# Kernel tuning notes

Measured on AMD Instinct MI355X. Metric: run time of the kernel, lower is better.

The kernel has to match this reference:

```python
import jax, jax.numpy as jnp
from jax import lax
import numpy as np

HEADS = 8

def _hswish(x):
    return x * jnp.clip(x + 3.0, 0.0, 6.0) / 6.0

def _sep_conv(x, dw, pw, pad):
    # depthwise conv (groups=C) followed by 1x1 pointwise conv, no bias
    dn = ('NCHW', 'OIHW', 'NCHW')
    y = lax.conv_general_dilated(x, dw, (1, 1), [(pad, pad), (pad, pad)],
                                 dimension_numbers=dn, feature_group_count=x.shape[1])
    return lax.conv_general_dilated(y, pw, (1, 1), [(0, 0), (0, 0)], dimension_numbers=dn)

def _bn(x, g, b, m, v):
    # SyncBatchNorm in eval mode (running stats), eps=1e-5
    inv = g / jnp.sqrt(v + 1e-5)
    return (x - m[:, None, None]) * inv[:, None, None] + b[:, None, None]

def _gn(x, g, b, groups=2):
    B, C, H, W = x.shape
    xg = x.reshape(B, groups, -1)
    mu = xg.mean(-1, keepdims=True)
    var = xg.var(-1, keepdims=True)
    xg = (xg - mu) / jnp.sqrt(var + 1e-5)
    return xg.reshape(B, C, H, W) * g[:, None, None] + b[:, None, None]

def _ln(x, g, b):
    mu = x.mean(-1, keepdims=True)
    var = x.var(-1, keepdims=True)
    return (x - mu) / jnp.sqrt(var + 1e-5) * g + b

def _forward(fl, h, w):
    (x, ln_q_g, ln_q_b, ln_k_g, ln_k_b, ln_v_g, ln_v_b, w_q, w_k, w_v, w_proj, b_proj,
     dw0, pw0, gn_g, gn_b, dw1, pw1, dw2, pw2,
     bn0_g, bn0_b, bn0_m, bn0_v, bn1_g, bn1_b, bn1_m, bn1_v, bn2_g, bn2_b, bn2_m, bn2_v) = fl
    B, C, N = x.shape  # C = attr_num tokens, N = dim = h*w
    d = N // HEADS
    scale = d ** -0.5
    q = _ln(x, ln_q_g, ln_q_b) @ w_q.T
    k = _ln(x, ln_k_g, ln_k_b) @ w_k.T
    v = _ln(x, ln_v_g, ln_v_b) @ w_v.T

    def agg(t):
        # aggregator(t.transpose(1,2), (h,w)) then head split; net input is (B,C,h,w)
        img = t.reshape(B, C, h, w)
        p0, p1, p2, p3 = jnp.split(img, 4, axis=1)  # seg_dim = C//4
        x0 = _hswish(_bn(p0, bn0_g, bn0_b, bn0_m, bn0_v))
        x1 = _hswish(_bn(_sep_conv(p1, dw1, pw1, 1), bn1_g, bn1_b, bn1_m, bn1_v))
        x2 = _hswish(_bn(_sep_conv(p2, dw2, pw2, 2), bn2_g, bn2_b, bn2_m, bn2_v))
        xl = _hswish(_gn(_sep_conv(p3, dw0, pw0, 1), gn_g, gn_b))
        y = jnp.concatenate([x0, x1, x2, xl], axis=1).reshape(B, C, N)
        return y.reshape(B, C, HEADS, d).transpose(0, 2, 1, 3)  # (B,H,C,d)

    qh, kh, vh = agg(q), agg(k), agg(v)
    scores = jnp.einsum('bhcd,bhkd->bhck', qh, kh)
    attn = jax.nn.softmax(jax.nn.gelu(scores, approximate=False) * scale, axis=-1)
    out = jnp.einsum('bhck,bhkd->bhcd', attn, vh).reshape(B, C, N)  # raw reshape as in torch
    out = out @ w_proj.T + b_proj
    out = out / jnp.maximum(jnp.linalg.norm(out, axis=-1, keepdims=True), 1e-12)
    return out, attn


def setup_inputs() -> dict:
    key = jax.random.key(0)
    ks = jax.random.split(key, 12)
    B, C, N = 32, 312, 1024
    sd = C // 4  # 78
    f32 = jnp.float32
    rn = lambda k, shp, s: jax.random.normal(k, shp, f32) * s
    inp = {
        'x': rn(ks[0], (B, C, N), 1.0),
        'h': 32, 'w': 32,
        'ln_q_g': jnp.ones((N,), f32), 'ln_q_b': jnp.zeros((N,), f32),
        'ln_k_g': jnp.ones((N,), f32), 'ln_k_b': jnp.zeros((N,), f32),
        'ln_v_g': jnp.ones((N,), f32), 'ln_v_b': jnp.zeros((N,), f32),
        'w_q': rn(ks[1], (N, N), N ** -0.5),
        'w_k': rn(ks[2], (N, N), N ** -0.5),
        'w_v': rn(ks[3], (N, N), N ** -0.5),
        'w_proj': rn(ks[4], (N, N), N ** -0.5),
        'b_proj': jnp.zeros((N,), f32),
        'dw0': rn(ks[5], (sd, 1, 3, 3), 1.0 / 3.0),
        'pw0': rn(ks[6], (sd, sd, 1, 1), sd ** -0.5),
        'gn_g': jnp.ones((sd,), f32), 'gn_b': jnp.zeros((sd,), f32),
        'dw1': rn(ks[7], (sd, 1, 3, 3), 1.0 / 3.0),
        'pw1': rn(ks[8], (sd, sd, 1, 1), sd ** -0.5),
        'dw2': rn(ks[9], (sd, 1, 5, 5), 1.0 / 5.0),
        'pw2': rn(ks[10], (sd, sd, 1, 1), sd ** -0.5),
    }
    for i in range(3):
        inp[f'bn{i}_g'] = jnp.ones((sd,), f32)
        inp[f'bn{i}_b'] = jnp.zeros((sd,), f32)
        inp[f'bn{i}_m'] = jnp.zeros((sd,), f32)
        inp[f'bn{i}_v'] = jnp.ones((sd,), f32)
    return inp


def reference(x, h, w, ln_q_g, ln_q_b, ln_k_g, ln_k_b, ln_v_g, ln_v_b, w_q, w_k, w_v, w_proj, b_proj, dw0, pw0, gn_g, gn_b, dw1, pw1, dw2, pw2, bn0_g, bn0_b, bn0_m, bn0_v, bn1_g, bn1_b, bn1_m, bn1_v, bn2_g, bn2_b, bn2_m, bn2_v):
    fl = (x, ln_q_g, ln_q_b, ln_k_g, ln_k_b, ln_v_g, ln_v_b, w_q, w_k, w_v, w_proj, b_proj,
          dw0, pw0, gn_g, gn_b, dw1, pw1, dw2, pw2,
          bn0_g, bn0_b, bn0_m, bn0_v, bn1_g, bn1_b, bn1_m, bn1_v, bn2_g, bn2_b, bn2_m, bn2_v)
    return _forward(fl, h, w)
```

## Files before the change

### kernel.cpp

```cpp
#include <hip/hip_runtime.h>
#include <hip/hip_bf16.h>
#include <float.h>

typedef __hip_bfloat16 bf16;
typedef __attribute__((ext_vector_type(8))) __bf16 bfrag;
typedef __attribute__((ext_vector_type(4))) float f32x4;

#define B_ 32
#define C_ 312
#define N_ 1024
#define H_ 8
#define D_ 128
#define SD_ 78
#define BC_ (B_ * C_)
#define BH_ (B_ * H_)

__device__ __forceinline__ float bf2f(bf16 x) { return __bfloat162float(x); }
__device__ __forceinline__ bf16 f2bf(float x) { return __float2bfloat16(x); }
__device__ __forceinline__ float hswish(float x) {
    return x * fminf(fmaxf(x + 3.0f, 0.0f), 6.0f) * (1.0f / 6.0f);
}

__device__ __forceinline__ void gload_lds16(const void* g, void* l) {
    __builtin_amdgcn_global_load_lds(
        (const __attribute__((address_space(1))) void*)g,
        (__attribute__((address_space(3))) void*)l, 16, 0, 0);
}

__global__ void ln_kernel(const float* __restrict__ x, bf16* __restrict__ xn) {
    int r = blockIdx.x;
    int t = threadIdx.x;
    const float* xr = x + (size_t)r * N_;
    float4 v4 = *reinterpret_cast<const float4*>(xr + t * 4);
    float s = v4.x + v4.y + v4.z + v4.w;
    float sq = v4.x * v4.x + v4.y * v4.y + v4.z * v4.z + v4.w * v4.w;
    __shared__ float rs[256], rq[256];
    rs[t] = s; rq[t] = sq; __syncthreads();
    for (int o = 128; o > 0; o >>= 1) {
        if (t < o) { rs[t] += rs[t + o]; rq[t] += rq[t + o]; }
        __syncthreads();
    }
    float mu = rs[0] * (1.0f / N_);
    float var = rq[0] * (1.0f / N_) - mu * mu;
    float rstd = rsqrtf(var + 1e-5f);
    __bf16 o4[4] = { (__bf16)((v4.x - mu) * rstd), (__bf16)((v4.y - mu) * rstd),
                     (__bf16)((v4.z - mu) * rstd), (__bf16)((v4.w - mu) * rstd) };
    *reinterpret_cast<uint2*>(reinterpret_cast<__bf16*>(xn) + (size_t)r * N_ + t * 4) =
        *reinterpret_cast<const uint2*>(o4);
}

__global__ void wcvt_kernel(const float* __restrict__ wq, const float* __restrict__ wk,
                            const float* __restrict__ wv, const float* __restrict__ wp,
                            const float* __restrict__ gq, const float* __restrict__ bq,
                            const float* __restrict__ gk, const float* __restrict__ bk,
                            const float* __restrict__ gv, const float* __restrict__ bv_,
                            bf16* __restrict__ wqkv, float* __restrict__ bias3,
                            bf16* __restrict__ wpb) {
    int n = blockIdx.x;
    int t = threadIdx.x;
    int k4 = t * 4;
    const float* src; const float* G = nullptr; const float* Bv = nullptr;
    if (n < 1024)      { src = wq + (size_t)n * N_;          G = gq; Bv = bq; }
    else if (n < 2048) { src = wk + (size_t)(n - 1024) * N_; G = gk; Bv = bk; }
    else if (n < 3072) { src = wv + (size_t)(n - 2048) * N_; G = gv; Bv = bv_; }
    else               { src = wp + (size_t)(n - 3072) * N_; }
    float4 w4 = *reinterpret_cast<const float4*>(src + k4);
    if (G) {
        __bf16 o[4] = { (__bf16)(w4.x * G[k4]),     (__bf16)(w4.y * G[k4 + 1]),
                        (__bf16)(w4.z * G[k4 + 2]), (__bf16)(w4.w * G[k4 + 3]) };
        *reinterpret_cast<uint2*>(wqkv + (size_t)n * N_ + k4) = *reinterpret_cast<const uint2*>(o);
        float s = w4.x * Bv[k4] + w4.y * Bv[k4 + 1] + w4.z * Bv[k4 + 2] + w4.w * Bv[k4 + 3];
        __shared__ float rs[256];
        rs[t] = s; __syncthreads();
        for (int o2 = 128; o2 > 0; o2 >>= 1) {
            if (t < o2) rs[t] += rs[t + o2];
            __syncthreads();
        }
        if (t == 0) bias3[n] = rs[0];
    } else {
        __bf16 o[4] = { (__bf16)w4.x, (__bf16)w4.y, (__bf16)w4.z, (__bf16)w4.w };
        *reinterpret_cast<uint2*>(wpb + (size_t)(n - 3072) * N_ + k4) = *reinterpret_cast<const uint2*>(o);
    }
}

template <bool OUTF32>
__global__ __launch_bounds__(256) void mfma_gemm_bw(
        const bf16* __restrict__ A_,
        const bf16* __restrict__ Wb,
        const float* __restrict__ bias, int nTx,
        void* __restrict__ O0, void* __restrict__ O1, void* __restrict__ O2) {
    const int K = 1024, Nout = 1024;
    __shared__ __bf16 sA[128 * 64];
    __shared__ __bf16 sB[128 * 64];
    const __bf16* A = reinterpret_cast<const __bf16*>(A_);
    const __bf16* W = reinterpret_cast<const __bf16*>(Wb);

    int t = threadIdx.x;
    int lane = t & 63, wave = t >> 6;
    int wm = (wave >> 1) * 64, wn = (wave & 1) * 64;
    int quad = lane >> 4, l15 = lane & 15;

    int cpx = gridDim.x >> 3;
    int tile = (blockIdx.x & 7) * cpx + (blockIdx.x >> 3);
    int bx = tile % nTx, by = tile / nTx;
    int m0 = by * 128;
    int w0 = bx * 128;
    int which = bx >> 3;
    int n0 = (bx & 7) * 128;

    int rowLoc = wave * 8 + (lane >> 3);
    int c8s = (lane & 7) ^ (lane >> 3);
    const __bf16* gA = A + (size_t)(m0 + rowLoc) * K + c8s * 8;
    const __bf16* gW = W + (size_t)(w0 + rowLoc) * K + c8s * 8;

    f32x4 acc[4][4];
#pragma unroll
    for (int i = 0; i < 4; i++)
#pragma unroll
        for (int j = 0; j < 4; j++) acc[i][j] = (f32x4)(0.f);

    for (int kt = 0; kt < 16; kt++) {
        int k0 = kt * 64;
#pragma unroll
        for (int cc = 0; cc < 4; cc++) {
            gload_lds16(gA + (size_t)cc * 32 * K + k0, &sA[cc * 2048 + wave * 512]);
            gload_lds16(gW + (size_t)cc * 32 * K + k0, &sB[cc * 2048 + wave * 512]);
        }
        __syncthreads();
#pragma unroll
        for (int kk = 0; kk < 2; kk++) {
            bfrag af[4], bfr[4];
#pragma unroll
            for (int mt = 0; mt < 4; mt++) {
                int row = wm + mt * 16 + l15;
                af[mt] = *reinterpret_cast<const bfrag*>(
                    &sA[(row * 8 + ((kk * 4 + quad) ^ (row & 7))) * 8]);
            }
#pragma unroll
            for (int nt = 0; nt < 4; nt++) {
                int row = wn + nt * 16 + l15;
                bfr[nt] = *reinterpret_cast<const bfrag*>(
                    &sB[(row * 8 + ((kk * 4 + quad) ^ (row & 7))) * 8]);
            }
#pragma unroll
            for (int mt = 0; mt < 4; mt++)
#pragma unroll
                for (int nt = 0; nt < 4; nt++)
                    acc[mt][nt] = __builtin_amdgcn_mfma_f32_16x16x32_bf16(af[mt], bfr[nt], acc[mt][nt], 0, 0, 0);
        }
        __syncthreads();
    }
    void* Cout = which == 0 ? O0 : (which == 1 ? O1 : O2);
#pragma unroll
    for (int mt = 0; mt < 4; mt++) {
#pragma unroll
        for (int nt = 0; nt < 4; nt++) {
            int cloc = wn + nt * 16 + l15;
            float bb = bias ? bias[w0 + cloc] : 0.f;
            int col = n0 + cloc;
#pragma unroll
            for (int r = 0; r < 4; r++) {
                int row = m0 + wm + mt * 16 + quad * 4 + r;
                float v = acc[mt][nt][r] + bb;
                if (OUTF32) ((float*)Cout)[(size_t)row * Nout + col] = v;
                else        ((bf16*)Cout)[(size_t)row * Nout + col] = f2bf(v);
            }
        }
    }
}

__global__ void seg0_kernel(const bf16* __restrict__ t0, const bf16* __restrict__ t1,
                            const bf16* __restrict__ t2,
                            bf16* __restrict__ h0, bf16* __restrict__ h1,
                            bf16* __restrict__ h2,
                            const float* __restrict__ g, const float* __restrict__ b,
                            const float* __restrict__ m, const float* __restrict__ v) {
    int ti = blockIdx.y;
    const bf16* tin = ti == 0 ? t0 : (ti == 1 ? t1 : t2);
    bf16* th = ti == 0 ? h0 : (ti == 1 ? h1 : h2);
    int bc = blockIdx.x;
    int bi = bc / SD_, c = bc % SD_;
    float inv = g[c] * rsqrtf(v[c] + 1e-5f);
    float mm = m[c], bb = b[c];
    const __bf16* tp = reinterpret_cast<const __bf16*>(tin) + ((size_t)bi * C_ + c) * N_;
    __bf16* base = reinterpret_cast<__bf16*>(th) + (size_t)bi * H_ * C_ * D_;
    int n = threadIdx.x * 4;
    uint2 in2 = *reinterpret_cast<const uint2*>(tp + n);
    const __bf16* iv = reinterpret_cast<const __bf16*>(&in2);
    __bf16 o4[4];
#pragma unroll
    for (int j = 0; j < 4; j++)
        o4[j] = (__bf16)hswish(((float)iv[j] - mm) * inv + bb);
    *reinterpret_cast<uint2*>(&base[((n >> 7) * C_ + c) * D_ + (n & 127)]) =
        *reinterpret_cast<const uint2*>(o4);
}

template <int KS, int MODE>
__device__ __forceinline__ void dwpw_impl(
        char* uMem, float* sDwF, float* sWk,
        const bf16* __restrict__ tin, int cOff,
        const float* __restrict__ dw, const float* __restrict__ pw,
        const float* __restrict__ g, const float* __restrict__ b,
        const float* __restrict__ m, const float* __restrict__ v,
        bf16* __restrict__ th, float* __restrict__ rawOut,
        int r0, int bi, int tid) {
    constexpr int WKP = ((KS * KS + 3) / 4) * 4;
    __bf16* sIn = reinterpret_cast<__bf16*>(uMem);
    float (*sWt)[80] = reinterpret_cast<float (*)[80]>(uMem);
    const int P = KS / 2;

    for (int u = tid; u < SD_ * KS * 2; u += 512) {
        int rowi = u >> 1, side = u & 1;
        *reinterpret_cast<uint2*>(sIn + rowi * 40 + (side ? 36 : 0)) = make_uint2(0u, 0u);
    }
    const __bf16* tbase = reinterpret_cast<const __bf16*>(tin) + ((size_t)bi * C_ + cOff) * N_;
    for (int u = tid; u < SD_ * KS * 4; u += 512) {
        int c = u / (KS * 4);
        int rem = u - c * (KS * 4);
        int di = rem >> 2, cb = rem & 3;
        int ii = r0 + di - P;
        uint4 val = make_uint4(0u, 0u, 0u, 0u);
        if (ii >= 0 && ii <= 31)
            val = *reinterpret_cast<const uint4*>(tbase + (size_t)c * N_ + ii * 32 + cb * 8);
        __bf16* dst = sIn + (c * KS + di) * 40 + 4 + cb * 8;
        *reinterpret_cast<uint2*>(dst)     = make_uint2(val.x, val.y);
        *reinterpret_cast<uint2*>(dst + 4) = make_uint2(val.z, val.w);
    }
    for (int i = tid; i < SD_ * KS * KS; i += 512) {
        int c = i / (KS * KS), q = i - c * (KS * KS);
        sWk[c * WKP + q] = dw[i];
    }
    __syncthreads();

    for (int u = tid; u < SD_ * 4; u += 512) {
        int c = u >> 2, q8 = (u & 3) << 3;
        const __bf16* rbase = sIn + (size_t)(c * KS) * 40;
        __bf16 rowv[KS][16];
#pragma unroll
        for (int di = 0; di < KS; di++) {
            *reinterpret_cast<bfrag*>(&rowv[di][0]) = *reinterpret_cast<const bfrag*>(rbase + di * 40 + q8);
            *reinterpret_cast<bfrag*>(&rowv[di][8]) = *reinterpret_cast<const bfrag*>(rbase + di * 40 + q8 + 8);
        }
        float wreg[WKP];
#pragma unroll
        for (int qq = 0; qq < WKP / 4; qq++)
            *reinterpret_cast<float4*>(&wreg[qq * 4]) =
                *reinterpret_cast<const float4*>(&sWk[c * WKP + qq * 4]);
        float acc8[8];
#pragma unroll
        for (int k = 0; k < 8; k++) acc8[k] = 0.f;
#pragma unroll
        for (int di = 0; di < KS; di++) {
#pragma unroll
            for (int dj = 0; dj < KS; dj++) {
                float w = wreg[di * KS + dj];
#pragma unroll
                for (int k = 0; k < 8; k++)
                    acc8[k] += (float)rowv[di][k + dj - P + 4] * w;
            }
        }
        *reinterpret_cast<float4*>(&sDwF[c * 32 + q8])     = *reinterpret_cast<const float4*>(&acc8[0]);
        *reinterpret_cast<float4*>(&sDwF[c * 32 + q8 + 4]) = *reinterpret_cast<const float4*>(&acc8[4]);
    }
    __syncthreads();

    for (int i = tid; i < SD_ * 80; i += 512) {
        int c = i / 80, o = i - c * 80;
        sWt[c][o] = (o < SD_) ? pw[o * SD_ + c] : 0.f;
    }
    __syncthreads();

    int p = tid & 31, og = tid >> 5;
    int o0 = og * 5;
    int no = (og == 15) ? 3 : 5;
    float acc[5];
#pragma unroll
    for (int i = 0; i < 5; i++) acc[i] = 0.f;
    for (int c = 0; c < SD_; c++) {
        float vv = sDwF[c * 32 + p];
#pragma unroll
        for (int q = 0; q < 5; q++)
            acc[q] += sWt[c][o0 + q] * vv;
    }
    int n = r0 * 32 + p;
    if (MODE == 0) {
        bf16* base = th + (size_t)bi * H_ * C_ * D_;
        for (int j = 0; j < no; j++) {
            int o = o0 + j;
            float inv = g[o] * rsqrtf(v[o] + 1e-5f);
            float y = hswish((acc[j] - m[o]) * inv + b[o]);
            base[((n >> 7) * C_ + cOff + o) * D_ + (n & 127)] = f2bf(y);
        }
    } else {
        float* opr = rawOut + (size_t)bi * SD_ * N_;
        for (int j = 0; j < no; j++)
            opr[(size_t)(o0 + j) * N_ + n] = acc[j];
    }
}

__global__ __launch_bounds__(512) void dwpw_all_kernel(
        const bf16* __restrict__ t0, const bf16* __restrict__ t1,
        const bf16* __restrict__ t2,
        const float* __restrict__ dw1, const float* __restrict__ pw1,
        const float* __restrict__ g1, const float* __restrict__ b1,
        const float* __restrict__ m1, const float* __restrict__ v1,
        const float* __restrict__ dw2, const float* __restrict__ pw2,
        const float* __restrict__ g2, const float* __restrict__ b2,
        const float* __restrict__ m2, const float* __restrict__ v2,
        const float* __restrict__ dw0, const float* __restrict__ pw0,
        bf16* __restrict__ h0, bf16* __restrict__ h1, bf16* __restrict__ h2,
        float* __restrict__ r0_, float* __restrict__ r1_, float* __restrict__ r2_) {
    __shared__ __align__(16) char uMem[SD_ * 5 * 40 * sizeof(__bf16)];
    __shared__ __align__(16) float sDwF[SD_ * 32];
    __shared__ __align__(16) float sWk[SD_ * 28];

    int ti = blockIdx.y;
    const bf16* tin = ti == 0 ? t0 : (ti == 1 ? t1 : t2);
    bf16* th = ti == 0 ? h0 : (ti == 1 ? h1 : h2);
    float* rawOut = ti == 0 ? r0_ : (ti == 1 ? r1_ : r2_);
    int r0 = blockIdx.x & 31;
    int bi = blockIdx.x >> 5;
    int tid = threadIdx.x;
    int branch = blockIdx.z;

    if (branch == 0) {
        dwpw_impl<3, 0>(uMem, sDwF, sWk, tin, SD_, dw1, pw1, g1, b1, m1, v1,
                        th, (float*)nullptr, r0, bi, tid);
    } else if (branch == 1) {
        dwpw_impl<5, 0>(uMem, sDwF, sWk, tin, 2 * SD_, dw2, pw2, g2, b2, m2, v2,
                        th, (float*)nullptr, r0, bi, tid);
    } else {
        dwpw_impl<3, 1>(uMem, sDwF, sWk, tin, 3 * SD_, dw0, pw0,
                        (const float*)nullptr, (const float*)nullptr,
                        (const float*)nullptr, (const float*)nullptr,
                        (bf16*)nullptr, rawOut, r0, bi, tid);
    }
}

__global__ void gn_stats_kernel(const float* __restrict__ r0_, const float* __restrict__ r1_,
                                const float* __restrict__ r2_, float* __restrict__ stats) {
    int ti = blockIdx.y;
    const float* tmp2 = ti == 0 ? r0_ : (ti == 1 ? r1_ : r2_);
    int bg = blockIdx.x;
    int bi = bg >> 1, grp = bg & 1;
    const float* p = tmp2 + (size_t)bi * SD_ * N_ + (size_t)grp * 39 * N_;
    float s = 0.f, sq = 0.f;
    const int TOT = 39 * N_;
    for (int i = threadIdx.x * 4; i < TOT; i += 1024) {
        float4 f4 = *reinterpret_cast<const float4*>(p + i);
        s += f4.x + f4.y + f4.z + f4.w;
        sq += f4.x * f4.x + f4.y * f4.y + f4.z * f4.z + f4.w * f4.w;
    }
    __shared__ float rs[256], rq[256];
    rs[threadIdx.x] = s; rq[threadIdx.x] = sq; __syncthreads();
    for (int o = 128; o > 0; o >>= 1) {
        if (threadIdx.x < o) { rs[threadIdx.x] += rs[threadIdx.x + o]; rq[threadIdx.x] += rq[threadIdx.x + o]; }
        __syncthreads();
    }
    if (threadIdx.x == 0) {
        float mu = rs[0] / (float)TOT;
        float var = rq[0] / (float)TOT - mu * mu;
        stats[ti * 128 + bg * 2] = mu;
        stats[ti * 128 + bg * 2 + 1] = rsqrtf(var + 1e-5f);
    }
}

__global__ void gn_apply_kernel(const float* __restrict__ r0_, const float* __restrict__ r1_,
                                const float* __restrict__ r2_, const float* __restrict__ stats,
                                const float* __restrict__ gg, const float* __restrict__ gb,
                                bf16* __restrict__ h0, bf16* __restrict__ h1,
                                bf16* __restrict__ h2) {
    int ti = blockIdx.y;
    const float* tmp2 = ti == 0 ? r0_ : (ti == 1 ? r1_ : r2_);
    bf16* th = ti == 0 ? h0 : (ti == 1 ? h1 : h2);
    int bc = blockIdx.x;
    int bi = bc / SD_, c = bc % SD_;
    int grp = c / 39;
    float mu = stats[ti * 128 + (bi * 2 + grp) * 2];
    float rstd = stats[ti * 128 + (bi * 2 + grp) * 2 + 1];
    float sc = gg[c] * rstd;
    float of = gb[c] - mu * sc;
    const float* p = tmp2 + ((size_t)bi * SD_ + c) * N_;
    __bf16* base = reinterpret_cast<__bf16*>(th) + (size_t)bi * H_ * C_ * D_;
    int n = threadIdx.x * 4;
    float4 f4 = *reinterpret_cast<const float4*>(p + n);
    __bf16 o4[4] = { (__bf16)hswish(f4.x * sc + of), (__bf16)hswish(f4.y * sc + of),
                     (__bf16)hswish(f4.z * sc + of), (__bf16)hswish(f4.w * sc + of) };
    *reinterpret_cast<uint2*>(&base[((n >> 7) * C_ + 234 + c) * D_ + (n & 127)]) =
        *reinterpret_cast<const uint2*>(o4);
}

#define SLDA 136
#define PLDA 328
__global__ __launch_bounds__(512, 4) void attn_av_kernel(
        const bf16* __restrict__ qh_, const bf16* __restrict__ kh_,
        const bf16* __restrict__ vh_,
        float* __restrict__ attnOut, bf16* __restrict__ ctx) {
    __shared__ __align__(16) char uni[60928];
    __shared__ float smax[64][2];
    __shared__ float ssum[64][2];
    __bf16* sQ = reinterpret_cast<__bf16*>(uni);
    __bf16* sK = reinterpret_cast<__bf16*>(uni + 17408);
    __bf16* sP = reinterpret_cast<__bf16*>(uni);
    __bf16* sV = reinterpret_cast<__bf16*>(uni + 41984);
    const __bf16* qh = reinterpret_cast<const __bf16*>(qh_);
    const __bf16* kh = reinterpret_cast<const __bf16*>(kh_);
    const __bf16* vh = reinterpret_cast<const __bf16*>(vh_);

    int strip = blockIdx.x;
    int bh = blockIdx.y;
    int t = threadIdx.x;
    int lane = t & 63, wave = t >> 6;
    int quad = lane >> 4, l15 = lane & 15;
    int wm = wave >> 1;
    int wn = wave & 1;

#pragma unroll
    for (int cc = 0; cc < 2; cc++) {
        int c = t + cc * 512;
        int row = c >> 4, seg = c & 15;
        int src = strip * 64 + row; if (src > 311) src = 311;
        bfrag v = *reinterpret_cast<const bfrag*>(qh + ((size_t)bh * C_ + src) * D_ + seg * 8);
        *reinterpret_cast<bfrag*>(&sQ[row * SLDA + seg * 8]) = v;
    }

    f32x4 acc[10];
#pragma unroll
    for (int i = 0; i < 10; i++) acc[i] = (f32x4)(0.f);

    bfrag af[4];
    bool afLoaded = false;

    for (int half = 0; half < 2; half++) {
        if (half) __syncthreads();
        for (int cc = 0; cc < 5; cc++) {
            int c = t + cc * 512;
            int row = c >> 4, seg = c & 15;
            int src = half * 160 + row;
            bfrag v;
            if (src < C_) {
                v = *reinterpret_cast<const bfrag*>(kh + ((size_t)bh * C_ + src) * D_ + seg * 8);
            } else {
#pragma unroll
                for (int j = 0; j < 8; j++) v[j] = (__bf16)0.f;
            }
            *reinterpret_cast<bfrag*>(&sK[row * SLDA + seg * 8]) = v;
        }
        __syncthreads();
        if (!afLoaded) {
#pragma unroll
            for (int ks = 0; ks < 4; ks++)
                af[ks] = *reinterpret_cast<const bfrag*>(&sQ[(wm * 16 + l15) * SLDA + ks * 32 + quad * 8]);
            afLoaded = true;
        }
#pragma unroll
        for (int ks = 0; ks < 4; ks++) {
#pragma unroll
            for (int jj = 0; jj < 5; jj++) {
                int lr = (wn * 5 + jj) * 16 + l15;
                bfrag bf = *reinterpret_cast<const bfrag*>(&sK[lr * SLDA + ks * 32 + quad * 8]);
                acc[half * 5 + jj] = __builtin_amdgcn_mfma_f32_16x16x32_bf16(af[ks], bf, acc[half * 5 + jj], 0, 0, 0);
            }
        }
    }

    const float scale = 0.08838834764831845f;
    const float inv_sqrt2 = 0.7071067811865475f;
#pragma unroll
    for (int a = 0; a < 10; a++) {
        int gt = (a / 5) * 10 + wn * 5 + (a % 5);
        int col = gt * 16 + l15;
#pragma unroll
        for (int r = 0; r < 4; r++) {
            float v = acc[a][r];
            float ge = 0.5f * v * (1.0f + erff(v * inv_sqrt2));
            float s = ge * scale;
            if (col >= C_) s = -FLT_MAX;
            acc[a][r] = s;
        }
    }
    float mx[4];
#pragma unroll
    for (int r = 0; r < 4; r++) {
        float m = -FLT_MAX;
#pragma unroll
        for (int a = 0; a < 10; a++) m = fmaxf(m, acc[a][r]);
        for (int o = 1; o < 16; o <<= 1) m = fmaxf(m, __shfl_xor(m, o));
        mx[r] = m;
    }
    if (l15 == 0) {
#pragma unroll
        for (int r = 0; r < 4; r++) smax[wm * 16 + quad * 4 + r][wn] = mx[r];
    }
    __syncthreads();
    float sm[4];
#pragma unroll
    for (int r = 0; r < 4; r++) {
        int row = wm * 16 + quad * 4 + r;
        float m = fmaxf(smax[row][0], smax[row][1]);
        float s = 0.f;
#pragma unroll
        for (int a = 0; a < 10; a++) {
            float e = __expf(acc[a][r] - m);
            acc[a][r] = e;
            s += e;
        }
        for (int o = 1; o < 16; o <<= 1) s += __shfl_xor(s, o);
        sm[r] = s;
    }
    if (l15 == 0) {
#pragma unroll
        for (int r = 0; r < 4; r++) ssum[wm * 16 + quad * 4 + r][wn] = sm[r];
    }
    __syncthreads();

#pragma unroll
    for (int r = 0; r < 4; r++) {
        int row = wm * 16 + quad * 4 + r;
        float inv = 1.0f / (ssum[row][0] + ssum[row][1]);
        int grow = strip * 64 + row;
        float* ao = attnOut + ((size_t)bh * C_ + grow) * C_;
#pragma unroll
        for (int a = 0; a < 10; a++) {
            int gt = (a / 5) * 10 + wn * 5 + (a % 5);
            int col = gt * 16 + l15;
            float pv = acc[a][r] * inv;
            if (grow < C_ && col < C_) ao[col] = pv;
            sP[row * PLDA + col] = f2bf(pv);
        }
    }

    f32x4 acc2[4];
#pragma unroll
    for (int i = 0; i < 4; i++) acc2[i] = (f32x4)(0.f);

    auto stageV = [&](int chunk) {
#pragma unroll
        for (int it = 0; it < 2; it++) {
            int g = t + it * 512;
            int d = g & 127;
            int oct = g >> 7;
            int ktl = oct >> 2, quad2 = oct & 3;
            int cb = chunk * 64 + ktl * 32 + quad2 * 8;
            const __bf16* vp = vh + ((size_t)bh * C_ + cb) * D_ + d;
            bfrag v;
            if (cb + 7 < C_) {
#pragma unroll
                for (int j = 0; j < 8; j++) v[j] = vp[(size_t)j * D_];
            } else {
#pragma unroll
                for (int j = 0; j < 8; j++) v[j] = (cb + j < C_) ? vp[(size_t)j * D_] : (__bf16)0.f;
            }
            *reinterpret_cast<bfrag*>(&sV[(((ktl * 8 + (d >> 4)) * 64) + quad2 * 16 + (d & 15)) * 8]) = v;
        }
    };

    stageV(0);
    __syncthreads();

    for (int chunk = 0; chunk < 5; chunk++) {
#pragma unroll
        for (int ktl = 0; ktl < 2; ktl++) {
            bfrag a = *reinterpret_cast<const bfrag*>(
                &sP[(wm * 16 + l15) * PLDA + chunk * 64 + ktl * 32 + quad * 8]);
#pragma unroll
            for (int ntl = 0; ntl < 4; ntl++) {
                int ntg = wn * 4 + ntl;
                bfrag b = *reinterpret_cast<const bfrag*>(&sV[(((ktl * 8 + ntg) * 64) + lane) * 8]);
                acc2[ntl] = __builtin_amdgcn_mfma_f32_16x16x32_bf16(a, b, acc2[ntl], 0, 0, 0);
            }
        }
        if (chunk < 4) {
            __syncthreads();
            stageV(chunk + 1);
            __syncthreads();
        }
    }

    int b = bh >> 3, h = bh & 7;
#pragma unroll
    for (int ntl = 0; ntl < 4; ntl++) {
        int d = wn * 64 + ntl * 16 + l15;
#pragma unroll
        for (int r = 0; r < 4; r++) {
            int c = strip * 64 + wm * 16 + quad * 4 + r;
            if (c < C_) {
                size_t oi = ((size_t)b * C_ + h * 39 + (c >> 3)) * N_ + ((c & 7) << 7) + d;
                ctx[oi] = f2bf(acc2[ntl][r]);
            }
        }
    }
}

__global__ void norm_kernel(const float* __restrict__ out3, float* __restrict__ outp) {
    int r = blockIdx.x;
    const float* p = out3 + (size_t)r * N_;
    float4 f4 = *reinterpret_cast<const float4*>(p + threadIdx.x * 4);
    float sq = f4.x * f4.x + f4.y * f4.y + f4.z * f4.z + f4.w * f4.w;
    __shared__ float rq[256];
    rq[threadIdx.x] = sq; __syncthreads();
    for (int o = 128; o > 0; o >>= 1) {
        if (threadIdx.x < o) rq[threadIdx.x] += rq[threadIdx.x + o];
        __syncthreads();
    }
    float inv = 1.0f / fmaxf(sqrtf(rq[0]), 1e-12f);
    float4 o4 = { f4.x * inv, f4.y * inv, f4.z * inv, f4.w * inv };
    *reinterpret_cast<float4*>(outp + (size_t)r * N_ + threadIdx.x * 4) = o4;
}

extern "C" void kernel_launch(void* const* d_in, const int* in_sizes, int n_in,
                              void* d_out, int out_size, void* d_ws, size_t ws_size,
                              hipStream_t stream) {
    const float* x      = (const float*)d_in[0];
    const float* ln_q_g = (const float*)d_in[3];
    const float* ln_q_b = (const float*)d_in[4];
    const float* ln_k_g = (const float*)d_in[5];
    const float* ln_k_b = (const float*)d_in[6];
    const float* ln_v_g = (const float*)d_in[7];
    const float* ln_v_b = (const float*)d_in[8];
    const float* w_q    = (const float*)d_in[9];
    const float* w_k    = (const float*)d_in[10];
    const float* w_v    = (const float*)d_in[11];
    const float* w_proj = (const float*)d_in[12];
    const float* b_proj = (const float*)d_in[13];
    const float* dw0    = (const float*)d_in[14];
    const float* pw0    = (const float*)d_in[15];
    const float* gn_g   = (const float*)d_in[16];
    const float* gn_b   = (const float*)d_in[17];
    const float* dw1    = (const float*)d_in[18];
    const float* pw1    = (const float*)d_in[19];
    const float* dw2    = (const float*)d_in[20];
    const float* pw2    = (const float*)d_in[21];
    const float* bn0_g  = (const float*)d_in[22];
    const float* bn0_b  = (const float*)d_in[23];
    const float* bn0_m  = (const float*)d_in[24];
    const float* bn0_v  = (const float*)d_in[25];
    const float* bn1_g  = (const float*)d_in[26];
    const float* bn1_b  = (const float*)d_in[27];
    const float* bn1_m  = (const float*)d_in[28];
    const float* bn1_v  = (const float*)d_in[29];
    const float* bn2_g  = (const float*)d_in[30];
    const float* bn2_b  = (const float*)d_in[31];
    const float* bn2_m  = (const float*)d_in[32];
    const float* bn2_v  = (const float*)d_in[33];

    char* ws = (char*)d_ws;
    size_t off = 0;
    auto alloc = [&](size_t bytes) {
        void* p = ws + off;
        off = (off + bytes + 255) & ~(size_t)255;
        return p;
    };
    const size_t BF_BYTES = (size_t)BC_ * N_ * sizeof(bf16);
    const size_t T2_FLOATS = (size_t)B_ * SD_ * N_;
    bf16*  xn   = (bf16*)alloc(BF_BYTES);
    bf16*  qb   = (bf16*)alloc(BF_BYTES);
    bf16*  kb   = (bf16*)alloc(BF_BYTES);
    bf16*  vb   = (bf16*)alloc(BF_BYTES);
    float* tmp2 = (float*)alloc(3 * T2_FLOATS * sizeof(float));
    float* gnst = (float*)alloc(2048);
    bf16*  wqkv = (bf16*)alloc((size_t)3 * N_ * N_ * sizeof(bf16));
    float* bias3 = (float*)alloc((size_t)3 * N_ * sizeof(float));
    bf16*  wpb  = (bf16*)alloc((size_t)N_ * N_ * sizeof(bf16));

    float* out_main = (float*)d_out;
    float* attn_out = out_main + (size_t)BC_ * N_;

    bf16* qh  = xn;
    bf16* kh  = (bf16*)out_main;
    bf16* vh  = kh + (size_t)BC_ * N_;
    bf16* ctx = vb;
    float* out3 = (float*)qb;
    float* r0 = tmp2, *r1 = tmp2 + T2_FLOATS, *r2 = tmp2 + 2 * T2_FLOATS;

    hipLaunchKernelGGL(wcvt_kernel, dim3(4096), dim3(256), 0, stream,
                       w_q, w_k, w_v, w_proj,
                       ln_q_g, ln_q_b, ln_k_g, ln_k_b, ln_v_g, ln_v_b,
                       wqkv, bias3, wpb);
    hipLaunchKernelGGL(ln_kernel, dim3(BC_), dim3(256), 0, stream, x, xn);
    hipLaunchKernelGGL((mfma_gemm_bw<false>), dim3(24 * 78), dim3(256), 0, stream,
                       xn, wqkv, bias3, 24, (void*)qb, (void*)kb, (void*)vb);

    hipLaunchKernelGGL(seg0_kernel, dim3(B_ * SD_, 3), dim3(256), 0, stream,
                       qb, kb, vb, qh, kh, vh, bn0_g, bn0_b, bn0_m, bn0_v);
    hipLaunchKernelGGL(dwpw_all_kernel, dim3(B_ * 32, 3, 3), dim3(512), 0, stream,
                       qb, kb, vb,
                       dw1, pw1, bn1_g, bn1_b, bn1_m, bn1_v,
                       dw2, pw2, bn2_g, bn2_b, bn2_m, bn2_v,
                       dw0, pw0,
                       qh, kh, vh, r0, r1, r2);
    hipLaunchKernelGGL(gn_stats_kernel, dim3(B_ * 2, 3), dim3(256), 0, stream,
                       r0, r1, r2, gnst);
    hipLaunchKernelGGL(gn_apply_kernel, dim3(B_ * SD_, 3), dim3(256), 0, stream,
                       r0, r1, r2, gnst, gn_g, gn_b, qh, kh, vh);

    hipLaunchKernelGGL(attn_av_kernel, dim3(5, BH_), dim3(512), 0, stream,
                       qh, kh, vh, attn_out, ctx);
    hipLaunchKernelGGL((mfma_gemm_bw<true>), dim3(8 * 78), dim3(256), 0, stream,
                       ctx, wpb, b_proj, 8, (void*)out3, (void*)out3, (void*)out3);
    hipLaunchKernelGGL(norm_kernel, dim3(BC_), dim3(256), 0, stream, out3, out_main);
}
```

Baseline: 633.7 us.

## Use bf16 MFMA for pointwise conv and process two rows per block

```diff
diff --git a/kernel.cpp b/kernel.cpp
--- a/kernel.cpp
+++ b/kernel.cpp
@@ -197,32 +197,37 @@
 
 template <int KS, int MODE>
 __device__ __forceinline__ void dwpw_impl(
-        char* uMem, float* sDwF, float* sWk,
+        char* uMem, float* sWk, __bf16* dwT,
         const bf16* __restrict__ tin, int cOff,
         const float* __restrict__ dw, const float* __restrict__ pw,
         const float* __restrict__ g, const float* __restrict__ b,
         const float* __restrict__ m, const float* __restrict__ v,
         bf16* __restrict__ th, float* __restrict__ rawOut,
-        int r0, int bi, int tid) {
+        int strip, int bi, int tid) {
     constexpr int WKP = ((KS * KS + 3) / 4) * 4;
+    constexpr int NR  = KS + 1;
     __bf16* sIn = reinterpret_cast<__bf16*>(uMem);
-    float (*sWt)[80] = reinterpret_cast<float (*)[80]>(uMem);
+    __bf16* sWm = reinterpret_cast<__bf16*>(uMem);
     const int P = KS / 2;
 
-    for (int u = tid; u < SD_ * KS * 2; u += 512) {
+    for (int u = tid; u < SD_ * NR * 2; u += 512) {
         int rowi = u >> 1, side = u & 1;
         *reinterpret_cast<uint2*>(sIn + rowi * 40 + (side ? 36 : 0)) = make_uint2(0u, 0u);
     }
+    for (int u = tid; u < 64 * 9; u += 512) {
+        int pos = u / 9, cc = 78 + (u % 9) * 2;
+        *reinterpret_cast<unsigned int*>(dwT + pos * 96 + cc) = 0u;
+    }
     const __bf16* tbase = reinterpret_cast<const __bf16*>(tin) + ((size_t)bi * C_ + cOff) * N_;
-    for (int u = tid; u < SD_ * KS * 4; u += 512) {
-        int c = u / (KS * 4);
-        int rem = u - c * (KS * 4);
+    for (int u = tid; u < SD_ * NR * 4; u += 512) {
+        int c = u / (NR * 4);
+        int rem = u - c * (NR * 4);
         int di = rem >> 2, cb = rem & 3;
-        int ii = r0 + di - P;
+        int ii = 2 * strip + di - P;
         uint4 val = make_uint4(0u, 0u, 0u, 0u);
         if (ii >= 0 && ii <= 31)
             val = *reinterpret_cast<const uint4*>(tbase + (size_t)c * N_ + ii * 32 + cb * 8);
-        __bf16* dst = sIn + (c * KS + di) * 40 + 4 + cb * 8;
+        __bf16* dst = sIn + (c * NR + di) * 40 + 4 + cb * 8;
         *reinterpret_cast<uint2*>(dst)     = make_uint2(val.x, val.y);
         *reinterpret_cast<uint2*>(dst + 4) = make_uint2(val.z, val.w);
     }
@@ -232,9 +237,10 @@
     }
     __syncthreads();
 
-    for (int u = tid; u < SD_ * 4; u += 512) {
-        int c = u >> 2, q8 = (u & 3) << 3;
-        const __bf16* rbase = sIn + (size_t)(c * KS) * 40;
+    for (int u = tid; u < SD_ * 8; u += 512) {
+        int c = u >> 3, grp = u & 7;
+        int row = grp >> 2, q8 = (grp & 3) << 3;
+        const __bf16* rbase = sIn + (size_t)(c * NR + row) * 40;
         __bf16 rowv[KS][16];
 #pragma unroll
         for (int di = 0; di < KS; di++) {
@@ -259,42 +265,67 @@
                     acc8[k] += (float)rowv[di][k + dj - P + 4] * w;
             }
         }
-        *reinterpret_cast<float4*>(&sDwF[c * 32 + q8])     = *reinterpret_cast<const float4*>(&acc8[0]);
-        *reinterpret_cast<float4*>(&sDwF[c * 32 + q8 + 4]) = *reinterpret_cast<const float4*>(&acc8[4]);
+#pragma unroll
+        for (int k = 0; k < 8; k++)
+            dwT[(row * 32 + q8 + k) * 96 + c] = (__bf16)acc8[k];
     }
     __syncthreads();
 
-    for (int i = tid; i < SD_ * 80; i += 512) {
-        int c = i / 80, o = i - c * 80;
-        sWt[c][o] = (o < SD_) ? pw[o * SD_ + c] : 0.f;
+    for (int u = tid; u < 80 * 96; u += 512) {
+        int o = u / 96, c = u - o * 96;
+        float val = (o < SD_ && c < SD_) ? pw[o * SD_ + c] : 0.f;
+        sWm[u] = (__bf16)val;
     }
     __syncthreads();
 
-    int p = tid & 31, og = tid >> 5;
-    int o0 = og * 5;
-    int no = (og == 15) ? 3 : 5;
-    float acc[5];
-#pragma unroll
-    for (int i = 0; i < 5; i++) acc[i] = 0.f;
-    for (int c = 0; c < SD_; c++) {
-        float vv = sDwF[c * 32 + p];
-#pragma unroll
-        for (int q = 0; q < 5; q++)
-            acc[q] += sWt[c][o0 + q] * vv;
-    }
-    int n = r0 * 32 + p;
+    int lane = tid & 63, wave = tid >> 6;
+    int quad = lane >> 4, l15 = lane & 15;
+    int wn = wave & 3, mh = wave >> 2;
+    int mt0 = mh ? 3 : 0;
+    int mcnt = mh ? 2 : 3;
+    f32x4 acc[3];
+#pragma unroll
+    for (int i = 0; i < 3; i++) acc[i] = (f32x4)(0.f);
+#pragma unroll
+    for (int kk = 0; kk < 3; kk++) {
+        bfrag bv = *reinterpret_cast<const bfrag*>(dwT + (wn * 16 + l15) * 96 + kk * 32 + quad * 8);
+#pragma unroll
+        for (int mi = 0; mi < 3; mi++) {
+            if (mi < mcnt) {
+                bfrag av = *reinterpret_cast<const bfrag*>(sWm + ((mt0 + mi) * 16 + l15) * 96 + kk * 32 + quad * 8);
+                acc[mi] = __builtin_amdgcn_mfma_f32_16x16x32_bf16(av, bv, acc[mi], 0, 0, 0);
+            }
+        }
+    }
+    int n = strip * 64 + wn * 16 + l15;
     if (MODE == 0) {
         bf16* base = th + (size_t)bi * H_ * C_ * D_;
-        for (int j = 0; j < no; j++) {
-            int o = o0 + j;
-            float inv = g[o] * rsqrtf(v[o] + 1e-5f);
-            float y = hswish((acc[j] - m[o]) * inv + b[o]);
-            base[((n >> 7) * C_ + cOff + o) * D_ + (n & 127)] = f2bf(y);
+#pragma unroll
+        for (int mi = 0; mi < 3; mi++) {
+            if (mi < mcnt) {
+#pragma unroll
+                for (int r = 0; r < 4; r++) {
+                    int o = (mt0 + mi) * 16 + quad * 4 + r;
+                    if (o < SD_) {
+                        float inv = g[o] * rsqrtf(v[o] + 1e-5f);
+                        float y = hswish((acc[mi][r] - m[o]) * inv + b[o]);
+                        base[((n >> 7) * C_ + cOff + o) * D_ + (n & 127)] = f2bf(y);
+                    }
+                }
+            }
         }
     } else {
         float* opr = rawOut + (size_t)bi * SD_ * N_;
-        for (int j = 0; j < no; j++)
-            opr[(size_t)(o0 + j) * N_ + n] = acc[j];
+#pragma unroll
+        for (int mi = 0; mi < 3; mi++) {
+            if (mi < mcnt) {
+#pragma unroll
+                for (int r = 0; r < 4; r++) {
+                    int o = (mt0 + mi) * 16 + quad * 4 + r;
+                    if (o < SD_) opr[(size_t)o * N_ + n] = acc[mi][r];
+                }
+            }
+        }
     }
 }
 
@@ -310,30 +341,30 @@
         const float* __restrict__ dw0, const float* __restrict__ pw0,
         bf16* __restrict__ h0, bf16* __restrict__ h1, bf16* __restrict__ h2,
         float* __restrict__ r0_, float* __restrict__ r1_, float* __restrict__ r2_) {
-    __shared__ __align__(16) char uMem[SD_ * 5 * 40 * sizeof(__bf16)];
-    __shared__ __align__(16) float sDwF[SD_ * 32];
+    __shared__ __align__(16) char uMem[SD_ * 6 * 40 * sizeof(__bf16)];
     __shared__ __align__(16) float sWk[SD_ * 28];
+    __shared__ __align__(16) __bf16 dwT[64 * 96];
 
     int ti = blockIdx.y;
     const bf16* tin = ti == 0 ? t0 : (ti == 1 ? t1 : t2);
     bf16* th = ti == 0 ? h0 : (ti == 1 ? h1 : h2);
     float* rawOut = ti == 0 ? r0_ : (ti == 1 ? r1_ : r2_);
-    int r0 = blockIdx.x & 31;
-    int bi = blockIdx.x >> 5;
+    int strip = blockIdx.x & 15;
+    int bi = blockIdx.x >> 4;
     int tid = threadIdx.x;
     int branch = blockIdx.z;
 
     if (branch == 0) {
-        dwpw_impl<3, 0>(uMem, sDwF, sWk, tin, SD_, dw1, pw1, g1, b1, m1, v1,
-                        th, (float*)nullptr, r0, bi, tid);
+        dwpw_impl<3, 0>(uMem, sWk, dwT, tin, SD_, dw1, pw1, g1, b1, m1, v1,
+                        th, (float*)nullptr, strip, bi, tid);
     } else if (branch == 1) {
-        dwpw_impl<5, 0>(uMem, sDwF, sWk, tin, 2 * SD_, dw2, pw2, g2, b2, m2, v2,
-                        th, (float*)nullptr, r0, bi, tid);
+        dwpw_impl<5, 0>(uMem, sWk, dwT, tin, 2 * SD_, dw2, pw2, g2, b2, m2, v2,
+                        th, (float*)nullptr, strip, bi, tid);
     } else {
-        dwpw_impl<3, 1>(uMem, sDwF, sWk, tin, 3 * SD_, dw0, pw0,
+        dwpw_impl<3, 1>(uMem, sWk, dwT, tin, 3 * SD_, dw0, pw0,
                         (const float*)nullptr, (const float*)nullptr,
                         (const float*)nullptr, (const float*)nullptr,
-                        (bf16*)nullptr, rawOut, r0, bi, tid);
+                        (bf16*)nullptr, rawOut, strip, bi, tid);
     }
 }
 
@@ -683,7 +714,7 @@
 
     hipLaunchKernelGGL(seg0_kernel, dim3(B_ * SD_, 3), dim3(256), 0, stream,
                        qb, kb, vb, qh, kh, vh, bn0_g, bn0_b, bn0_m, bn0_v);
-    hipLaunchKernelGGL(dwpw_all_kernel, dim3(B_ * 32, 3, 3), dim3(512), 0, stream,
+    hipLaunchKernelGGL(dwpw_all_kernel, dim3(B_ * 16, 3, 3), dim3(512), 0, stream,
                        qb, kb, vb,
                        dw1, pw1, bn1_g, bn1_b, bn1_m, bn1_v,
                        dw2, pw2, bn2_g, bn2_b, bn2_m, bn2_v,
```

Measured after the change: 560.6 us. 11.5% less time.
